# Performance work log

Measured on AMD Instinct MI355X. Metric: run time of the kernel, lower is better.

The kernel has to match this reference:

```python
import jax, jax.numpy as jnp
import numpy as np


def ste_sign(x):
    # Binarize with straight-through estimator: forward sign(), backward identity
    return x + jax.lax.stop_gradient(jnp.sign(x) - x)


def conv(x, w):
    # 3x3 VALID conv, NCHW / OIHW
    return jax.lax.conv_general_dilated(
        x, w, window_strides=(1, 1), padding='VALID',
        dimension_numbers=('NCHW', 'OIHW', 'NCHW'))


def maxpool2(x):
    return jax.lax.reduce_window(
        x, -jnp.inf, jax.lax.max,
        window_dimensions=(1, 1, 2, 2), window_strides=(1, 1, 2, 2),
        padding='VALID')


def hardtanh(x):
    return jnp.clip(x, -1.0, 1.0)


_CHANNELS = [(3, 4), (4, 8), (8, 16), (16, 32), (32, 64), (64, 32), (32, 2)]


def setup_inputs() -> dict:
    key = jax.random.key(0)
    keys = jax.random.split(key, 8)
    inp = {'inputs': jax.random.normal(keys[0], (64, 3, 256, 256), dtype=jnp.float32)}
    for i, (cin, cout) in enumerate(_CHANNELS):
        fan_in = cin * 9
        inp[f'w{i}'] = jax.random.normal(keys[i + 1], (cout, cin, 3, 3), dtype=jnp.float32) / np.sqrt(fan_in)
    return inp


def reference(inputs, w0, w1, w2, w3, w4, w5, w6):
    ws = [w0, w1, w2, w3, w4, w5, w6]
    x = inputs
    for i, w in enumerate(ws):
        xin = x if i == 0 else ste_sign(x)  # first layer sees raw 3-channel input
        x = conv(xin, ste_sign(w))
        x = hardtanh(x)
        if i == 0:
            x = maxpool2(x)
    return x.reshape(x.shape[0], -1)
```

## Files before the change

### kernel.cpp

```cpp
#include <hip/hip_runtime.h>
#include <stdint.h>


#define DEVINL __device__ __forceinline__
typedef int i32x4 __attribute__((ext_vector_type(4)));

DEVINL int dot4(uint32_t a, uint32_t b, int c) {
#if __has_builtin(__builtin_amdgcn_sdot4)
    return __builtin_amdgcn_sdot4((int)a, (int)b, c, false);
#else
    #pragma unroll
    for (int i = 0; i < 4; ++i)
        c += (int)(int8_t)(a >> (8 * i)) * (int)(int8_t)(b >> (8 * i));
    return c;
#endif
}

DEVINL uint32_t clampb(int v) {
    v = v > 1 ? 1 : (v < -1 ? -1 : v);
    return (uint32_t)(uint8_t)(int8_t)v;
}

__global__ __launch_bounds__(256) void conv0_pool_sign(
    const float* __restrict__ x, const float* __restrict__ w,
    uint32_t* __restrict__ out)
{
    __shared__ float ws[108];
    const int t = threadIdx.x;
    if (t < 108) {
        float v = w[t];
        ws[t] = (v > 0.f) ? 1.f : ((v < 0.f) ? -1.f : 0.f);
    }
    __syncthreads();
    const int idx = blockIdx.x * 256 + t;
    if (idx >= 64 * 127 * 127) return;
    const int px = idx % 127;
    const int py = (idx / 127) % 127;
    const int n  = idx / (127 * 127);

    double acc[4][4];
    #pragma unroll
    for (int co = 0; co < 4; ++co)
        #pragma unroll
        for (int p = 0; p < 4; ++p) acc[co][p] = 0.0;

    for (int ci = 0; ci < 3; ++ci) {
        float patch[4][4];
        const float* xp = x + (((size_t)n * 3 + ci) * 256 + 2 * py) * 256 + 2 * px;
        #pragma unroll
        for (int r = 0; r < 4; ++r) {
            const float2* q = (const float2*)(xp + r * 256);
            float2 p01 = q[0], p23 = q[1];
            patch[r][0] = p01.x; patch[r][1] = p01.y;
            patch[r][2] = p23.x; patch[r][3] = p23.y;
        }
        #pragma unroll
        for (int co = 0; co < 4; ++co) {
            const float* wsc = &ws[co * 27 + ci * 9];
            #pragma unroll
            for (int ky = 0; ky < 3; ++ky)
                #pragma unroll
                for (int kx = 0; kx < 3; ++kx) {
                    const double wv = (double)wsc[ky * 3 + kx];
                    acc[co][0] += (double)patch[ky][kx]         * wv;
                    acc[co][1] += (double)patch[ky][kx + 1]     * wv;
                    acc[co][2] += (double)patch[ky + 1][kx]     * wv;
                    acc[co][3] += (double)patch[ky + 1][kx + 1] * wv;
                }
        }
    }
    uint32_t u = 0;
    #pragma unroll
    for (int co = 0; co < 4; ++co) {
        const double m = fmax(fmax(acc[co][0], acc[co][1]), fmax(acc[co][2], acc[co][3]));
        const uint32_t s = (m > 0.0) ? 1u : ((m < 0.0) ? 0xFFu : 0u);
        u |= s << (8 * co);
    }
    out[idx] = u;
}

__global__ __launch_bounds__(256) void conv_l1(
    const uint32_t* __restrict__ in, const float* __restrict__ w,
    uint2* __restrict__ out)
{
    __shared__ uint32_t pw[72];
    const int t = threadIdx.x;
    if (t < 72) {
        const int co = t / 9, tap = t % 9;
        uint32_t u = 0;
        #pragma unroll
        for (int ci = 0; ci < 4; ++ci) {
            float v = w[(co * 4 + ci) * 9 + tap];
            uint32_t s = (v > 0.f) ? 1u : ((v < 0.f) ? 0xFFu : 0u);
            u |= s << (8 * ci);
        }
        pw[t] = u;
    }
    __syncthreads();

    const int idx = blockIdx.x * 256 + t;
    const int xg  = idx & 31;
    const int rest = idx >> 5;
    const int py  = rest % 125;
    const int n   = rest / 125;
    int px0 = xg * 4; if (px0 > 121) px0 = 121;

    const uint32_t* base = in + ((size_t)(n * 127 + py) * 127 + px0);
    uint32_t d[3][6];
    #pragma unroll
    for (int r = 0; r < 3; ++r)
        #pragma unroll
        for (int c = 0; c < 6; ++c)
            d[r][c] = base[r * 127 + c];

    int acc[4][8];
    #pragma unroll
    for (int j = 0; j < 4; ++j)
        #pragma unroll
        for (int co = 0; co < 8; ++co) acc[j][co] = 0;

    #pragma unroll
    for (int ky = 0; ky < 3; ++ky)
        #pragma unroll
        for (int kx = 0; kx < 3; ++kx) {
            const int tap = ky * 3 + kx;
            #pragma unroll
            for (int co = 0; co < 8; ++co) {
                const uint32_t wv = pw[co * 9 + tap];
                #pragma unroll
                for (int j = 0; j < 4; ++j)
                    acc[j][co] = dot4(d[ky][j + kx], wv, acc[j][co]);
            }
        }

    uint2* orow = out + ((size_t)(n * 125 + py) * 125 + px0);
    #pragma unroll
    for (int j = 0; j < 4; ++j) {
        uint32_t u0 = 0, u1 = 0;
        #pragma unroll
        for (int co = 0; co < 4; ++co) u0 |= clampb(acc[j][co]) << (8 * co);
        #pragma unroll
        for (int co = 0; co < 4; ++co) u1 |= clampb(acc[j][co + 4]) << (8 * co);
        orow[j] = make_uint2(u0, u1);
    }
}

__global__ __launch_bounds__(256) void conv_l2(
    const uint32_t* __restrict__ in, const float* __restrict__ w,
    i32x4* __restrict__ out)
{
    __shared__ uint32_t pw[288];
    const int t = threadIdx.x;
    for (int i = t; i < 288; i += 256) {
        const int co = i / 18, r = i % 18, tap = r / 2, half = r % 2;
        uint32_t u = 0;
        #pragma unroll
        for (int ci = 0; ci < 4; ++ci) {
            float v = w[(co * 8 + half * 4 + ci) * 9 + tap];
            uint32_t s = (v > 0.f) ? 1u : ((v < 0.f) ? 0xFFu : 0u);
            u |= s << (8 * ci);
        }
        pw[i] = u;
    }
    __syncthreads();

    const int idx = blockIdx.x * 256 + t;
    if (idx >= 64 * 123 * 31) return;
    const int xg   = idx % 31;
    const int rest = idx / 31;
    const int py   = rest % 123;
    const int n    = rest / 123;
    int px0 = xg * 4; if (px0 > 119) px0 = 119;

    const uint32_t* base = in + ((size_t)(n * 125 + py) * 125 + px0) * 2;
    uint32_t d[3][6][2];
    #pragma unroll
    for (int r = 0; r < 3; ++r)
        #pragma unroll
        for (int c = 0; c < 6; ++c) {
            d[r][c][0] = base[(r * 125 + c) * 2];
            d[r][c][1] = base[(r * 125 + c) * 2 + 1];
        }

    int acc[4][16];
    #pragma unroll
    for (int j = 0; j < 4; ++j)
        #pragma unroll
        for (int co = 0; co < 16; ++co) acc[j][co] = 0;

    #pragma unroll
    for (int ky = 0; ky < 3; ++ky)
        #pragma unroll
        for (int kx = 0; kx < 3; ++kx) {
            const int tap = ky * 3 + kx;
            #pragma unroll
            for (int co = 0; co < 16; ++co) {
                const uint32_t w0 = pw[(co * 9 + tap) * 2];
                const uint32_t w1 = pw[(co * 9 + tap) * 2 + 1];
                #pragma unroll
                for (int j = 0; j < 4; ++j)
                    acc[j][co] = dot4(d[ky][j + kx][1], w1,
                                 dot4(d[ky][j + kx][0], w0, acc[j][co]));
            }
        }

    i32x4* orow = out + ((size_t)(n * 123 + py) * 123 + px0);
    #pragma unroll
    for (int j = 0; j < 4; ++j) {
        uint32_t u[4];
        #pragma unroll
        for (int q = 0; q < 4; ++q) {
            u[q] = 0;
            #pragma unroll
            for (int b = 0; b < 4; ++b)
                u[q] |= clampb(acc[j][q * 4 + b]) << (8 * b);
        }
        orow[j] = (i32x4){(int)u[0], (int)u[1], (int)u[2], (int)u[3]};
    }
}

__global__ __launch_bounds__(256) void prepack_w(
    const float* __restrict__ w3, const float* __restrict__ w4,
    const float* __restrict__ w5, const float* __restrict__ w6,
    int8_t* __restrict__ pA)
{
    const int idx = blockIdx.x * 256 + threadIdx.x;
    const float* w; int CIN, COUT, MTILES, NMF, off;
    if      (idx < 6144)  { w = w3; CIN = 16; COUT = 32; MTILES = 2; NMF = 3; off = 0; }
    else if (idx < 26624) { w = w4; CIN = 32; COUT = 64; MTILES = 2; NMF = 5; off = 6144; }
    else if (idx < 45056) { w = w5; CIN = 64; COUT = 32; MTILES = 2; NMF = 9; off = 26624; }
    else if (idx < 50176) { w = w6; CIN = 32; COUT = 2;  MTILES = 1; NMF = 5; off = 45056; }
    else return;
    const int TP = 64 / CIN;
    const int s   = idx - off;
    const int per = MTILES * NMF * 1024;
    const int cg  = s / per;
    const int rem = s % per;
    const int mt  = rem / (NMF * 1024);
    const int r2  = rem % (NMF * 1024);
    const int f   = r2 >> 10;
    const int l   = (r2 >> 4) & 63;
    const int j   = r2 & 15;
    const int m   = l & 15;
    const int g   = l >> 4;
    const int k   = g * 16 + j;
    const int tap = f * TP + k / CIN;
    const int ci  = k % CIN;
    const int co  = cg * (16 * MTILES) + mt * 16 + m;
    int8_t v = 0;
    if (tap < 9 && co < COUT) {
        float x = w[((size_t)co * CIN + ci) * 9 + tap];
        v = (x > 0.f) ? (int8_t)1 : ((x < 0.f) ? (int8_t)(-1) : (int8_t)0);
    }
    pA[idx] = v;
}

template <int CIN, int COUT, int MTILES, int CGW, int R, int WI, bool FOUT>
__global__ __launch_bounds__(64 * R * CGW) void conv_mfma(
    const int8_t* __restrict__ in, const int8_t* __restrict__ packA,
    void* __restrict__ outp, int Wo)
{
    constexpr int TP  = 64 / CIN;
    constexpr int NMF = (9 + TP - 1) / TP;
    constexpr int NP  = CIN / 16;
    constexpr int CB  = 66;
    constexpr int NT  = 64 * R * CGW;
    constexpr int SR  = R + 2;
    constexpr int NU  = (SR * CB + NT - 1) / NT;
    __shared__ __align__(16) int8_t lds[NP * SR * CB * 16];

    const int t  = threadIdx.x;
    const int n  = blockIdx.z;
    const int by = blockIdx.y >> 1;
    const int bx = blockIdx.y & 1;
    const int y0 = by * R;
    const int f0 = bx * 4;
    const int cbase = f0 * 16;
    const int ncols = (WI - cbase < CB) ? (WI - cbase) : CB;
    const int npx   = SR * ncols;

    const int8_t* nin = in + (size_t)n * WI * WI * CIN;
    i32x4 st[NU][NP];
    #pragma unroll
    for (int u = 0; u < NU; ++u) {
        int p  = t + u * NT;
        int pp = p < npx ? p : npx - 1;
        int row  = pp / ncols;
        int col  = cbase + pp % ncols;
        int grow = y0 + row; if (grow > WI - 1) grow = WI - 1;
        const int8_t* src = nin + ((size_t)grow * WI + col) * CIN;
        #pragma unroll
        for (int pl = 0; pl < NP; ++pl)
            st[u][pl] = *(const i32x4*)(src + pl * 16);
    }

    const int l = t & 63, wv = t >> 6, g = l >> 4, npix = l & 15;
    const int cgw  = (CGW == 2 && wv >= R) ? 1 : 0;
    const int wrow = wv - cgw * R;
    i32x4 a[MTILES][NMF];
    {
        const int8_t* ap = packA + (size_t)cgw * MTILES * NMF * 1024 + l * 16;
        #pragma unroll
        for (int mt = 0; mt < MTILES; ++mt)
            #pragma unroll
            for (int f = 0; f < NMF; ++f)
                a[mt][f] = *(const i32x4*)(ap + (mt * NMF + f) * 1024);
    }

    #pragma unroll
    for (int u = 0; u < NU; ++u) {
        int p = t + u * NT;
        if (p < npx) {
            int row = p / ncols, colrel = p % ncols;
            #pragma unroll
            for (int pl = 0; pl < NP; ++pl)
                *(i32x4*)&lds[(size_t)(pl * SR * CB + row * CB + colrel) * 16] = st[u][pl];
        }
    }
    __syncthreads();

    const int y = y0 + wrow;
    if (y >= Wo) return;

    const int gdiv  = (g * 16) / CIN;
    const int plane = ((g * 16) % CIN) / 16;
    int loff[NMF];
    #pragma unroll
    for (int f = 0; f < NMF; ++f) {
        int tap = f * TP + gdiv;
        if (tap > 8) tap = 8;
        loff[f] = (plane * SR * CB + (wrow + tap / 3) * CB + (tap % 3) + npix) << 4;
    }

    #pragma unroll
    for (int i = 0; i < 4; ++i) {
        int x0 = (f0 + i) * 16;
        if (x0 > Wo - 16) x0 = Wo - 16;
        const int xrel = x0 - cbase;

        i32x4 bv[NMF];
        #pragma unroll
        for (int f = 0; f < NMF; ++f)
            bv[f] = *(const i32x4*)&lds[loff[f] + (xrel << 4)];

        i32x4 acc[MTILES];
        #pragma unroll
        for (int mt = 0; mt < MTILES; ++mt) {
            acc[mt] = (i32x4){0, 0, 0, 0};
            #pragma unroll
            for (int f = 0; f < NMF; ++f)
                acc[mt] = __builtin_amdgcn_mfma_i32_16x16x64_i8(a[mt][f], bv[f], acc[mt], 0, 0, 0);
        }

        if (!FOUT) {
            uint8_t* orow = (uint8_t*)outp + ((size_t)n * Wo + y) * (size_t)Wo * COUT
                          + (size_t)(x0 + npix) * COUT
                          + cgw * (16 * MTILES) + (g << 2);
            #pragma unroll
            for (int mt = 0; mt < MTILES; ++mt) {
                uint32_t u = 0;
                #pragma unroll
                for (int rr = 0; rr < 4; ++rr)
                    u |= clampb(acc[mt][rr]) << (8 * rr);
                *(uint32_t*)(orow + mt * 16) = u;
            }
        } else {
            float* fo = (float*)outp;
            #pragma unroll
            for (int rr = 0; rr < 4; ++rr) {
                const int m = g * 4 + rr;
                if (m < COUT) {
                    int v = acc[0][rr];
                    v = v > 1 ? 1 : (v < -1 ? -1 : v);
                    fo[((size_t)(n * COUT + m) * Wo + y) * Wo + x0 + npix] = (float)v;
                }
            }
        }
    }
}

extern "C" void kernel_launch(void* const* d_in, const int* in_sizes, int n_in,
                              void* d_out, int out_size, void* d_ws, size_t ws_size,
                              hipStream_t stream) {
    const float* x  = (const float*)d_in[0];
    const float* w0 = (const float*)d_in[1];
    const float* w1 = (const float*)d_in[2];
    const float* w2 = (const float*)d_in[3];
    const float* w3 = (const float*)d_in[4];
    const float* w4 = (const float*)d_in[5];
    const float* w5 = (const float*)d_in[6];
    const float* w6 = (const float*)d_in[7];

    int8_t* A  = (int8_t*)d_ws;
    int8_t* B  = A + 58491136;
    int8_t* pA = B + 29984768;

    prepack_w<<<196, 256, 0, stream>>>(w3, w4, w5, w6, pA);

    conv0_pool_sign<<<4033, 256, 0, stream>>>(x, w0, (uint32_t*)A);
    conv_l1<<<1000, 256, 0, stream>>>((const uint32_t*)A, w1, (uint2*)B);
    conv_l2<<<954, 256, 0, stream>>>((const uint32_t*)B, w2, (i32x4*)A);

    conv_mfma<16, 32, 2, 1, 8, 123, false><<<dim3(1, 16 * 2, 64), 512, 0, stream>>>(A, pA + 0, B, 121);
    conv_mfma<32, 64, 2, 2, 4, 121, false><<<dim3(1, 30 * 2, 64), 512, 0, stream>>>(B, pA + 6144, A, 119);
    conv_mfma<64, 32, 1, 2, 4, 119, false><<<dim3(1, 30 * 2, 64), 512, 0, stream>>>(A, pA + 26624, B, 117);
    conv_mfma<32, 2, 1, 1, 4, 117, true ><<<dim3(1, 29 * 2, 64), 256, 0, stream>>>(B, pA + 45056, d_out, 115);
}
```

Measured before the change: 242.1 us.

## Switch MFMA conv layers to 32x32x32 int8 tiles with repacked weights

New measurement: 244.9 us. About the same (+1.2%).

```diff
diff --git a/kernel.cpp b/kernel.cpp
--- a/kernel.cpp
+++ b/kernel.cpp
@@ -3,7 +3,8 @@
 
 
 #define DEVINL __device__ __forceinline__
-typedef int i32x4 __attribute__((ext_vector_type(4)));
+typedef int i32x4  __attribute__((ext_vector_type(4)));
+typedef int i32x16 __attribute__((ext_vector_type(16)));
 
 DEVINL int dot4(uint32_t a, uint32_t b, int c) {
 #if __has_builtin(__builtin_amdgcn_sdot4)
@@ -225,28 +226,23 @@
     int8_t* __restrict__ pA)
 {
     const int idx = blockIdx.x * 256 + threadIdx.x;
-    const float* w; int CIN, COUT, MTILES, NMF, off;
-    if      (idx < 6144)  { w = w3; CIN = 16; COUT = 32; MTILES = 2; NMF = 3; off = 0; }
-    else if (idx < 26624) { w = w4; CIN = 32; COUT = 64; MTILES = 2; NMF = 5; off = 6144; }
-    else if (idx < 45056) { w = w5; CIN = 64; COUT = 32; MTILES = 2; NMF = 9; off = 26624; }
-    else if (idx < 50176) { w = w6; CIN = 32; COUT = 2;  MTILES = 1; NMF = 5; off = 45056; }
+    const float* w; int CIN, COUT, NMF, off;
+    if      (idx < 5120)  { w = w3; CIN = 16; COUT = 32; NMF = 5;  off = 0; }
+    else if (idx < 23552) { w = w4; CIN = 32; COUT = 64; NMF = 9;  off = 5120; }
+    else if (idx < 41984) { w = w5; CIN = 64; COUT = 32; NMF = 18; off = 23552; }
+    else if (idx < 51200) { w = w6; CIN = 32; COUT = 2;  NMF = 9;  off = 41984; }
     else return;
-    const int TP = 64 / CIN;
     const int s   = idx - off;
-    const int per = MTILES * NMF * 1024;
-    const int cg  = s / per;
-    const int rem = s % per;
-    const int mt  = rem / (NMF * 1024);
-    const int r2  = rem % (NMF * 1024);
+    const int ct  = s / (NMF * 1024);
+    const int r2  = s % (NMF * 1024);
     const int f   = r2 >> 10;
     const int l   = (r2 >> 4) & 63;
     const int j   = r2 & 15;
-    const int m   = l & 15;
-    const int g   = l >> 4;
-    const int k   = g * 16 + j;
-    const int tap = f * TP + k / CIN;
-    const int ci  = k % CIN;
-    const int co  = cg * (16 * MTILES) + mt * 16 + m;
+    const int np  = CIN / 16;
+    const int chunk = 2 * f + (l >> 5);
+    const int tap = chunk / np;
+    const int ci  = (chunk % np) * 16 + j;
+    const int co  = ct * 32 + (l & 31);
     int8_t v = 0;
     if (tap < 9 && co < COUT) {
         float x = w[((size_t)co * CIN + ci) * 9 + tap];
@@ -255,27 +251,27 @@
     pA[idx] = v;
 }
 
-template <int CIN, int COUT, int MTILES, int CGW, int R, int WI, bool FOUT>
-__global__ __launch_bounds__(64 * R * CGW) void conv_mfma(
+template <int CIN, int COUT, int CT, int R, int WI, bool FOUT>
+__global__ __launch_bounds__(64 * R) void conv_mfma(
     const int8_t* __restrict__ in, const int8_t* __restrict__ packA,
     void* __restrict__ outp, int Wo)
 {
-    constexpr int TP  = 64 / CIN;
-    constexpr int NMF = (9 + TP - 1) / TP;
     constexpr int NP  = CIN / 16;
+    constexpr int NMF = (9 * CIN + 31) / 32;
     constexpr int CB  = 66;
-    constexpr int NT  = 64 * R * CGW;
     constexpr int SR  = R + 2;
+    constexpr int PST = SR * CB * 16 + 16;
+    constexpr int NT  = 64 * R;
     constexpr int NU  = (SR * CB + NT - 1) / NT;
-    __shared__ __align__(16) int8_t lds[NP * SR * CB * 16];
+    constexpr int GRP = NMF > 9 ? 9 : NMF;
+    __shared__ __align__(16) int8_t lds[NP * PST];
 
     const int t  = threadIdx.x;
     const int n  = blockIdx.z;
     const int by = blockIdx.y >> 1;
     const int bx = blockIdx.y & 1;
     const int y0 = by * R;
-    const int f0 = bx * 4;
-    const int cbase = f0 * 16;
+    const int cbase = bx * 64;
     const int ncols = (WI - cbase < CB) ? (WI - cbase) : CB;
     const int npx   = SR * ncols;
 
@@ -294,17 +290,15 @@
             st[u][pl] = *(const i32x4*)(src + pl * 16);
     }
 
-    const int l = t & 63, wv = t >> 6, g = l >> 4, npix = l & 15;
-    const int cgw  = (CGW == 2 && wv >= R) ? 1 : 0;
-    const int wrow = wv - cgw * R;
-    i32x4 a[MTILES][NMF];
+    const int l = t & 63, wv = t >> 6, h = l >> 5, npix = l & 31;
+    i32x4 a[CT][NMF];
     {
-        const int8_t* ap = packA + (size_t)cgw * MTILES * NMF * 1024 + l * 16;
-        #pragma unroll
-        for (int mt = 0; mt < MTILES; ++mt)
+        const int8_t* ap = packA + l * 16;
+        #pragma unroll
+        for (int ct = 0; ct < CT; ++ct)
             #pragma unroll
             for (int f = 0; f < NMF; ++f)
-                a[mt][f] = *(const i32x4*)(ap + (mt * NMF + f) * 1024);
+                a[ct][f] = *(const i32x4*)(ap + (ct * NMF + f) * 1024);
     }
 
     #pragma unroll
@@ -314,65 +308,70 @@
             int row = p / ncols, colrel = p % ncols;
             #pragma unroll
             for (int pl = 0; pl < NP; ++pl)
-                *(i32x4*)&lds[(size_t)(pl * SR * CB + row * CB + colrel) * 16] = st[u][pl];
+                *(i32x4*)&lds[pl * PST + (row * CB + colrel) * 16] = st[u][pl];
         }
     }
     __syncthreads();
 
-    const int y = y0 + wrow;
+    const int y = y0 + wv;
     if (y >= Wo) return;
 
-    const int gdiv  = (g * 16) / CIN;
-    const int plane = ((g * 16) % CIN) / 16;
     int loff[NMF];
     #pragma unroll
     for (int f = 0; f < NMF; ++f) {
-        int tap = f * TP + gdiv;
+        const int chunk = 2 * f + h;
+        const int plane = chunk % NP;
+        int tap = chunk / NP;
         if (tap > 8) tap = 8;
-        loff[f] = (plane * SR * CB + (wrow + tap / 3) * CB + (tap % 3) + npix) << 4;
-    }
-
-    #pragma unroll
-    for (int i = 0; i < 4; ++i) {
-        int x0 = (f0 + i) * 16;
-        if (x0 > Wo - 16) x0 = Wo - 16;
-        const int xrel = x0 - cbase;
-
-        i32x4 bv[NMF];
-        #pragma unroll
-        for (int f = 0; f < NMF; ++f)
-            bv[f] = *(const i32x4*)&lds[loff[f] + (xrel << 4)];
-
-        i32x4 acc[MTILES];
-        #pragma unroll
-        for (int mt = 0; mt < MTILES; ++mt) {
-            acc[mt] = (i32x4){0, 0, 0, 0};
-            #pragma unroll
-            for (int f = 0; f < NMF; ++f)
-                acc[mt] = __builtin_amdgcn_mfma_i32_16x16x64_i8(a[mt][f], bv[f], acc[mt], 0, 0, 0);
+        loff[f] = plane * PST + (((wv + tap / 3) * CB + (tap % 3) + npix) << 4);
+    }
+
+    #pragma unroll
+    for (int i = 0; i < 2; ++i) {
+        int x0 = (bx * 2 + i) * 32;
+        if (x0 > Wo - 32) x0 = Wo - 32;
+        const int xrel16 = (x0 - cbase) << 4;
+
+        i32x16 acc[CT];
+        #pragma unroll
+        for (int ct = 0; ct < CT; ++ct)
+            acc[ct] = (i32x16){0,0,0,0,0,0,0,0,0,0,0,0,0,0,0,0};
+
+        #pragma unroll
+        for (int g0 = 0; g0 < NMF; g0 += GRP) {
+            i32x4 bv[GRP];
+            #pragma unroll
+            for (int f = 0; f < GRP; ++f)
+                bv[f] = *(const i32x4*)&lds[loff[g0 + f] + xrel16];
+            #pragma unroll
+            for (int f = 0; f < GRP; ++f)
+                #pragma unroll
+                for (int ct = 0; ct < CT; ++ct)
+                    acc[ct] = __builtin_amdgcn_mfma_i32_32x32x32_i8(
+                        a[ct][g0 + f], bv[f], acc[ct], 0, 0, 0);
         }
 
         if (!FOUT) {
-            uint8_t* orow = (uint8_t*)outp + ((size_t)n * Wo + y) * (size_t)Wo * COUT
-                          + (size_t)(x0 + npix) * COUT
-                          + cgw * (16 * MTILES) + (g << 2);
-            #pragma unroll
-            for (int mt = 0; mt < MTILES; ++mt) {
-                uint32_t u = 0;
-                #pragma unroll
-                for (int rr = 0; rr < 4; ++rr)
-                    u |= clampb(acc[mt][rr]) << (8 * rr);
-                *(uint32_t*)(orow + mt * 16) = u;
-            }
+            uint8_t* base = (uint8_t*)outp
+                          + (((size_t)n * Wo + y) * Wo + x0 + npix) * COUT + 4 * h;
+            #pragma unroll
+            for (int ct = 0; ct < CT; ++ct)
+                #pragma unroll
+                for (int q = 0; q < 4; ++q) {
+                    uint32_t u = clampb(acc[ct][4 * q + 0])
+                               | (clampb(acc[ct][4 * q + 1]) << 8)
+                               | (clampb(acc[ct][4 * q + 2]) << 16)
+                               | (clampb(acc[ct][4 * q + 3]) << 24);
+                    *(uint32_t*)(base + ct * 32 + 8 * q) = u;
+                }
         } else {
-            float* fo = (float*)outp;
-            #pragma unroll
-            for (int rr = 0; rr < 4; ++rr) {
-                const int m = g * 4 + rr;
-                if (m < COUT) {
-                    int v = acc[0][rr];
+            if (h == 0) {
+                float* fo = (float*)outp;
+                #pragma unroll
+                for (int r = 0; r < 2; ++r) {
+                    int v = acc[0][r];
                     v = v > 1 ? 1 : (v < -1 ? -1 : v);
-                    fo[((size_t)(n * COUT + m) * Wo + y) * Wo + x0 + npix] = (float)v;
+                    fo[((size_t)(n * COUT + r) * Wo + y) * Wo + x0 + npix] = (float)v;
                 }
             }
         }
@@ -395,14 +394,14 @@
     int8_t* B  = A + 58491136;
     int8_t* pA = B + 29984768;
 
-    prepack_w<<<196, 256, 0, stream>>>(w3, w4, w5, w6, pA);
+    prepack_w<<<200, 256, 0, stream>>>(w3, w4, w5, w6, pA);
 
     conv0_pool_sign<<<4033, 256, 0, stream>>>(x, w0, (uint32_t*)A);
     conv_l1<<<1000, 256, 0, stream>>>((const uint32_t*)A, w1, (uint2*)B);
     conv_l2<<<954, 256, 0, stream>>>((const uint32_t*)B, w2, (i32x4*)A);
 
-    conv_mfma<16, 32, 2, 1, 8, 123, false><<<dim3(1, 16 * 2, 64), 512, 0, stream>>>(A, pA + 0, B, 121);
-    conv_mfma<32, 64, 2, 2, 4, 121, false><<<dim3(1, 30 * 2, 64), 512, 0, stream>>>(B, pA + 6144, A, 119);
-    conv_mfma<64, 32, 1, 2, 4, 119, false><<<dim3(1, 30 * 2, 64), 512, 0, stream>>>(A, pA + 26624, B, 117);
-    conv_mfma<32, 2, 1, 1, 4, 117, true ><<<dim3(1, 29 * 2, 64), 256, 0, stream>>>(B, pA + 45056, d_out, 115);
-}
+    conv_mfma<16, 32, 1, 8, 123, false><<<dim3(1, 16 * 2, 64), 512, 0, stream>>>(A, pA + 0, B, 121);
+    conv_mfma<32, 64, 2, 4, 121, false><<<dim3(1, 30 * 2, 64), 256, 0, stream>>>(B, pA + 5120, A, 119);
+    conv_mfma<64, 32, 1, 4, 119, false><<<dim3(1, 30 * 2, 64), 256, 0, stream>>>(A, pA + 23552, B, 117);
+    conv_mfma<32, 2, 1, 4, 117, true ><<<dim3(1, 29 * 2, 64), 256, 0, stream>>>(B, pA + 41984, d_out, 115);
+}
```
